# Optimization experiments

Measured on AMD Instinct MI355X. Metric: run time of the kernel, lower is better.

Reference implementation:

```python
import jax, jax.numpy as jnp
import numpy as np
import math

NUM_HEADS = 8
NUM_CHANNELS = 512
B, C, H, W = 8, 512, 32, 32
LN_EPS = 1e-6


def setup_inputs() -> dict:
    key = jax.random.key(0)
    ks = jax.random.split(key, 7)
    s = 1.0 / math.sqrt(NUM_CHANNELS)
    return {
        "key": jax.random.normal(ks[0], (B, C, H, W), jnp.float32),
        "value": jax.random.normal(ks[1], (B, C, H, W), jnp.float32),
        "query": jax.random.normal(ks[2], (B, C, H, W), jnp.float32),
        "Wq": jax.random.normal(ks[3], (C, C), jnp.float32) * s,
        "Wk": jax.random.normal(ks[4], (C, C), jnp.float32) * s,
        "Wv": jax.random.normal(ks[5], (C, C), jnp.float32) * s,
        "Wo": jax.random.normal(ks[6], (C, C), jnp.float32) * s,
        "ln_gamma": jnp.ones((C,), jnp.float32),
        "ln_beta": jnp.zeros((C,), jnp.float32),
    }


def _to_tokens(x):
    # b c h w -> b (h w) c
    b, c, h, w = x.shape
    return x.transpose(0, 2, 3, 1).reshape(b, h * w, c)


def _split_heads(x, m):
    # (B, HW, C) -> (B, m, HW, d); matches reshape (B,HW,m,d) then 'b hw m d -> (b m) hw d'
    b, hw, c = x.shape
    d = c // m
    return x.reshape(b, hw, m, d).transpose(0, 2, 1, 3)


def _merge_heads_cm(x):
    # (B, m, HW, d) -> (B, HW, d*m) with channel index = c*m + head  ('(b m) hw c -> b hw (c m)')
    b, m, hw, d = x.shape
    return x.transpose(0, 2, 3, 1).reshape(b, hw, d * m)


def reference(key, value, query, Wq, Wk, Wv, Wo, ln_gamma, ln_beta):
    m = NUM_HEADS
    b, c, h, w = query.shape
    d = c // m

    q = _to_tokens(query) @ Wq.T  # (B, HW, C)
    k = _to_tokens(key) @ Wk.T
    v = _to_tokens(value) @ Wv.T

    qh = _split_heads(q, m)  # (B, m, HW, d)
    kh = _split_heads(k, m)
    vh = _split_heads(v, m)

    scores = jnp.einsum('bmqd,bmkd->bmqk', qh, kh) / math.sqrt(d)
    p_attn = jax.nn.softmax(scores, axis=-1)
    out = jnp.einsum('bmqk,bmkd->bmqd', p_attn, vh)  # (B, m, HW, d)

    out = _merge_heads_cm(out)        # (B, HW, C) interleaved as (c m)
    residual = _merge_heads_cm(qh)    # same interleaving of projected query

    x = out + residual
    mu = jnp.mean(x, axis=-1, keepdims=True)
    var = jnp.mean(jnp.square(x - mu), axis=-1, keepdims=True)
    x = (x - mu) / jnp.sqrt(var + LN_EPS) * ln_gamma + ln_beta

    x = x @ Wo.T  # (B, HW, C)
    return x.reshape(b, h, w, c).transpose(0, 3, 1, 2)  # b (h w) c -> b c h w
```

## Files before the change

### kernel.cpp

```cpp
#include <hip/hip_runtime.h>
#include <stdint.h>

typedef __bf16 bf16x8 __attribute__((ext_vector_type(8)));
typedef float f32x4 __attribute__((ext_vector_type(4)));
typedef unsigned short u16x4 __attribute__((ext_vector_type(4)));
typedef unsigned short u16x8 __attribute__((ext_vector_type(8)));

#define MFMA16(a, b, c) __builtin_amdgcn_mfma_f32_16x16x32_bf16(a, b, c, 0, 0, 0)

__device__ __forceinline__ unsigned short f2bf(float f) {
  union { float f; unsigned u; } v; v.f = f;
  unsigned r = v.u + 0x7fffu + ((v.u >> 16) & 1u);
  return (unsigned short)(r >> 16);
}
__device__ __forceinline__ float bf2f(unsigned short h) {
  union { unsigned u; float f; } v; v.u = ((unsigned)h) << 16; return v.f;
}
__device__ __forceinline__ unsigned pk2(float a, float b) {
  union { unsigned u; __bf16 h[2]; } v;
  v.h[0] = (__bf16)a;
  v.h[1] = (__bf16)b;
  return v.u;
}
__device__ __forceinline__ void gload16(const void* g, void* l) {
  __builtin_amdgcn_global_load_lds(
      (const __attribute__((address_space(1))) void*)g,
      (__attribute__((address_space(3))) void*)l, 16, 0, 0);
}
__device__ __forceinline__ float fexp2(float x) {
#if __has_builtin(__builtin_amdgcn_exp2f)
  return __builtin_amdgcn_exp2f(x);
#else
  return exp2f(x);
#endif
}

__global__ __launch_bounds__(256) void prep_kernel(
    const float* __restrict__ q, const float* __restrict__ k,
    const float* __restrict__ v, unsigned short* __restrict__ oq,
    unsigned short* __restrict__ ok, unsigned short* __restrict__ ov,
    const float* __restrict__ w0, const float* __restrict__ w1,
    const float* __restrict__ w2, const float* __restrict__ w3,
    unsigned short* __restrict__ y0, unsigned short* __restrict__ y1,
    unsigned short* __restrict__ y2, unsigned short* __restrict__ y3) {
  __shared__ float tile[64][33];
  int z = blockIdx.z;
  if (z == 3) {
    int idx = blockIdx.y * 32 + blockIdx.x;
    if (idx >= 512) return;
    int wsel = idx >> 7, xb = idx & 127;
    const float* s = wsel == 0 ? w0 : wsel == 1 ? w1 : wsel == 2 ? w2 : w3;
    unsigned short* d = wsel == 0 ? y0 : wsel == 1 ? y1 : wsel == 2 ? y2 : y3;
    int t = xb * 256 + threadIdx.x;
    const f32x4* sp = (const f32x4*)(s + (size_t)t * 8);
    f32x4 a = sp[0], b = sp[1];
    u16x8 r;
    r[0] = f2bf(a[0]); r[1] = f2bf(a[1]); r[2] = f2bf(a[2]); r[3] = f2bf(a[3]);
    r[4] = f2bf(b[0]); r[5] = f2bf(b[1]); r[6] = f2bf(b[2]); r[7] = f2bf(b[3]);
    *(u16x8*)(d + (size_t)t * 8) = r;
    return;
  }
  const float* src = z == 0 ? q : z == 1 ? k : v;
  unsigned short* dst = z == 0 ? oq : z == 1 ? ok : ov;
  int bb = blockIdx.y >> 3;
  int c0 = (blockIdx.y & 7) * 64;
  int t0 = blockIdx.x * 32;
  int tx = threadIdx.x & 31, r = threadIdx.x >> 5;
#pragma unroll
  for (int i = 0; i < 8; ++i)
    tile[r + i * 8][tx] = src[(size_t)(bb * 512 + c0 + r + i * 8) * 1024 + t0 + tx];
  __syncthreads();
#pragma unroll
  for (int i = 0; i < 4; ++i) {
    int tr = r + i * 8;
    unsigned pack = (unsigned)f2bf(tile[2 * tx][tr]) |
                    ((unsigned)f2bf(tile[2 * tx + 1][tr]) << 16);
    *(unsigned*)(dst + (size_t)(bb * 1024 + t0 + tr) * 512 + c0 + 2 * tx) = pack;
  }
}

__global__ __launch_bounds__(256, 4) void gemm_qkv(
    const unsigned short* __restrict__ A0, const unsigned short* __restrict__ A1,
    const unsigned short* __restrict__ A2,
    const unsigned short* __restrict__ B0, const unsigned short* __restrict__ B1,
    const unsigned short* __restrict__ B2,
    unsigned short* __restrict__ O0, unsigned short* __restrict__ O1,
    unsigned short* __restrict__ O2) {
  __shared__ unsigned short aT[2][128 * 32];
  __shared__ unsigned short bT[2][128 * 32];
  int z = blockIdx.y;
  const unsigned short* A = z == 0 ? A0 : z == 1 ? A1 : A2;
  const unsigned short* BT = z == 0 ? B0 : z == 1 ? B1 : B2;
  int j = blockIdx.x;
  int bm = (j & 7) * 8 + (j >> 5);
  int bn = (j >> 3) & 3;
  int tid = threadIdx.x, lane = tid & 63, w = tid >> 6;
  int wr = w >> 1, wc = w & 1, l15 = lane & 15, lhi = lane >> 4;
  const int m0 = bm * 128, n0 = bn * 128;

  int u0 = tid, u1 = 256 + tid;
  int ar0 = u0 >> 2, ac0 = (u0 & 3) ^ (ar0 & 3);
  int ar1 = u1 >> 2, ac1 = (u1 & 3) ^ (ar1 & 3);
  const unsigned short* asrc0 = A + (size_t)(m0 + ar0) * 512 + ac0 * 8;
  const unsigned short* asrc1 = A + (size_t)(m0 + ar1) * 512 + ac1 * 8;
  const unsigned short* bsrc0 = BT + (size_t)(n0 + ar0) * 512 + ac0 * 8;
  const unsigned short* bsrc1 = BT + (size_t)(n0 + ar1) * 512 + ac1 * 8;

#define QSTAGE(bufi, it)                                     \
  do {                                                       \
    gload16(asrc0 + (it) * 32, &aT[bufi][u0 * 8]);           \
    gload16(asrc1 + (it) * 32, &aT[bufi][u1 * 8]);           \
    gload16(bsrc0 + (it) * 32, &bT[bufi][u0 * 8]);           \
    gload16(bsrc1 + (it) * 32, &bT[bufi][u1 * 8]);           \
  } while (0)

  int aoff[4], boff[4];
#pragma unroll
  for (int i = 0; i < 4; ++i) {
    int arow = wr * 64 + i * 16 + l15;
    int brow = wc * 64 + i * 16 + l15;
    aoff[i] = arow * 32 + ((lhi ^ (arow & 3)) * 8);
    boff[i] = brow * 32 + ((lhi ^ (brow & 3)) * 8);
  }

  f32x4 acc[4][4] = {};

#define QTILE(BUF, IT)                                                        \
  do {                                                                       \
    if ((IT) + 1 < 16) QSTAGE((BUF) ^ 1, (IT) + 1);                           \
    bf16x8 af[4], bfr[4];                                                    \
    _Pragma("unroll") for (int mi = 0; mi < 4; ++mi)                          \
        af[mi] = *(const bf16x8*)&aT[BUF][aoff[mi]];                          \
    _Pragma("unroll") for (int ni = 0; ni < 4; ++ni)                          \
        bfr[ni] = *(const bf16x8*)&bT[BUF][boff[ni]];                         \
    __builtin_amdgcn_s_setprio(1);                                           \
    _Pragma("unroll") for (int mi = 0; mi < 4; ++mi)                          \
        _Pragma("unroll") for (int ni = 0; ni < 4; ++ni)                      \
            acc[mi][ni] = MFMA16(af[mi], bfr[ni], acc[mi][ni]);               \
    __builtin_amdgcn_s_setprio(0);                                           \
    __syncthreads();                                                         \
  } while (0)

  QSTAGE(0, 0);
  __syncthreads();
  for (int it2 = 0; it2 < 16; it2 += 2) {
    QTILE(0, it2);
    QTILE(1, it2 + 1);
  }
#undef QTILE
#undef QSTAGE

  float sc = (z == 1) ? (0.125f * 1.44269504f) : 1.0f;
#pragma unroll
  for (int mi = 0; mi < 4; ++mi) {
#pragma unroll
    for (int ni = 0; ni < 4; ++ni) {
      int row = m0 + wr * 64 + mi * 16 + lhi * 4;
      int col = n0 + wc * 64 + ni * 16 + l15;
      if (z < 2) {
        unsigned short* C = z == 0 ? O0 : O1;
#pragma unroll
        for (int j2 = 0; j2 < 4; ++j2)
          C[(size_t)(row + j2) * 512 + col] = f2bf(acc[mi][ni][j2] * sc);
      } else {
        int bb = row >> 10, hw = row & 1023;
        u16x4 p;
        p[0] = f2bf(acc[mi][ni][0]); p[1] = f2bf(acc[mi][ni][1]);
        p[2] = f2bf(acc[mi][ni][2]); p[3] = f2bf(acc[mi][ni][3]);
        *(u16x4*)&O2[(size_t)bb * 524288 + (size_t)col * 1024 + hw] = p;
      }
    }
  }
}

__global__ __launch_bounds__(256, 4) void gemm_out(const unsigned short* __restrict__ A,
                                                   const unsigned short* __restrict__ BT,
                                                   float* __restrict__ C) {
  __shared__ unsigned short aT[2][128 * 32];
  __shared__ unsigned short bT[2][64 * 32];
  int j = blockIdx.x;
  int bm = (j & 7) * 8 + (j >> 6);
  int bn = (j >> 3) & 7;
  int tid = threadIdx.x, lane = tid & 63, w = tid >> 6;
  int l15 = lane & 15, lhi = lane >> 4;
  const int m0 = bm * 128, n0 = bn * 64;

  int u0 = tid, u1 = 256 + tid;
  int ar0 = u0 >> 2, ac0 = (u0 & 3) ^ (ar0 & 3);
  int ar1 = u1 >> 2, ac1 = (u1 & 3) ^ (ar1 & 3);
  const unsigned short* asrc0 = A + (size_t)(m0 + ar0) * 512 + ac0 * 8;
  const unsigned short* asrc1 = A + (size_t)(m0 + ar1) * 512 + ac1 * 8;
  const unsigned short* bsrc0 = BT + (size_t)(n0 + ar0) * 512 + ac0 * 8;

#define OSTAGE(bufi, it)                                     \
  do {                                                       \
    gload16(asrc0 + (it) * 32, &aT[bufi][u0 * 8]);           \
    gload16(asrc1 + (it) * 32, &aT[bufi][u1 * 8]);           \
    gload16(bsrc0 + (it) * 32, &bT[bufi][u0 * 8]);           \
  } while (0)

  int aoff[2], boff[4];
#pragma unroll
  for (int i = 0; i < 2; ++i) {
    int arow = w * 32 + i * 16 + l15;
    aoff[i] = arow * 32 + ((lhi ^ (arow & 3)) * 8);
  }
#pragma unroll
  for (int i = 0; i < 4; ++i) {
    int brow = i * 16 + l15;
    boff[i] = brow * 32 + ((lhi ^ (brow & 3)) * 8);
  }

  f32x4 acc[2][4] = {};

#define OTILE(BUF, IT)                                                        \
  do {                                                                       \
    if ((IT) + 1 < 16) OSTAGE((BUF) ^ 1, (IT) + 1);                           \
    bf16x8 af[2], bfr[4];                                                    \
    _Pragma("unroll") for (int mi = 0; mi < 2; ++mi)                          \
        af[mi] = *(const bf16x8*)&aT[BUF][aoff[mi]];                          \
    _Pragma("unroll") for (int ni = 0; ni < 4; ++ni)                          \
        bfr[ni] = *(const bf16x8*)&bT[BUF][boff[ni]];                         \
    __builtin_amdgcn_s_setprio(1);                                           \
    _Pragma("unroll") for (int mi = 0; mi < 2; ++mi)                          \
        _Pragma("unroll") for (int ni = 0; ni < 4; ++ni)                      \
            acc[mi][ni] = MFMA16(af[mi], bfr[ni], acc[mi][ni]);               \
    __builtin_amdgcn_s_setprio(0);                                           \
    __syncthreads();                                                         \
  } while (0)

  OSTAGE(0, 0);
  __syncthreads();
  for (int it2 = 0; it2 < 16; it2 += 2) {
    OTILE(0, it2);
    OTILE(1, it2 + 1);
  }
#undef OTILE
#undef OSTAGE

#pragma unroll
  for (int mi = 0; mi < 2; ++mi) {
#pragma unroll
    for (int ni = 0; ni < 4; ++ni) {
      int row = m0 + w * 32 + mi * 16 + lhi * 4;
      int col = n0 + ni * 16 + l15;
      int bb = row >> 10, hw = row & 1023;
      *(f32x4*)&C[(size_t)bb * 524288 + (size_t)col * 1024 + hw] = acc[mi][ni];
    }
  }
}

__global__ __launch_bounds__(256, 2) void attn_kernel(
    const unsigned short* __restrict__ q_tok, const unsigned short* __restrict__ k_tok,
    const unsigned short* __restrict__ v_cm, unsigned short* __restrict__ y_hm) {
  __shared__ unsigned short k_lds[2][64 * 64];
  __shared__ unsigned short v_lds[2][64 * 64];
  __shared__ unsigned short p_lds[4][2][16 * 64];

  int bid = blockIdx.x;
  int slot = bid >> 3;
  int bh = (bid & 7) * 8 + (slot >> 3);
  int qb = slot & 7;
  int h = bh & 7, b = bh >> 3;
  int tid = threadIdx.x;
  int lane = tid & 63, w = tid >> 6;
  int l15 = lane & 15, lhi = lane >> 4;

  const unsigned short* kbase = k_tok + (size_t)b * 524288 + h * 64;
  const unsigned short* vbase = v_cm + (size_t)b * 524288 + (size_t)h * 65536;

  int qglob0 = b * 1024 + qb * 128 + w * 32;
  bf16x8 qf[2][2];
#pragma unroll
  for (int sub = 0; sub < 2; ++sub) {
    const unsigned short* qp =
        q_tok + (size_t)(qglob0 + sub * 16 + l15) * 512 + h * 64 + lhi * 8;
    qf[sub][0] = *(const bf16x8*)qp;
    qf[sub][1] = *(const bf16x8*)(qp + 32);
  }

  bf16x8 ones;
#pragma unroll
  for (int i = 0; i < 8; ++i) ones[i] = (__bf16)1.0f;

  int u0 = tid, u1 = 256 + tid;
  int r0 = u0 >> 3, c0 = (u0 & 7) ^ (r0 & 7);
  int r1 = u1 >> 3, c1 = (u1 & 7) ^ (r1 & 7);
  const unsigned short* ksrc0 = kbase + (size_t)r0 * 512 + c0 * 8;
  const unsigned short* ksrc1 = kbase + (size_t)r1 * 512 + c1 * 8;
  const unsigned short* vsrc0 = vbase + (size_t)r0 * 1024 + c0 * 8;
  const unsigned short* vsrc1 = vbase + (size_t)r1 * 1024 + c1 * 8;

#define STAGE(bufi, kti)                                                    \
  do {                                                                      \
    gload16(ksrc0 + (size_t)(kti) * 32768, &k_lds[bufi][u0 * 8]);           \
    gload16(ksrc1 + (size_t)(kti) * 32768, &k_lds[bufi][u1 * 8]);           \
    gload16(vsrc0 + (kti) * 64, &v_lds[bufi][u0 * 8]);                      \
    gload16(vsrc1 + (kti) * 64, &v_lds[bufi][u1 * 8]);                      \
  } while (0)

  int kvoff[4][2];
#pragma unroll
  for (int nt = 0; nt < 4; ++nt) {
    int brow = nt * 16 + l15, sw = brow & 7;
    kvoff[nt][0] = brow * 64 + ((lhi ^ sw) * 8);
    kvoff[nt][1] = brow * 64 + (((4 + lhi) ^ sw) * 8);
  }

  char* pb = (char*)&p_lds[w][0][0];
  int p2 = (l15 & 7) << 1;
  char* pwr[2][4];
  const char* prd[2][2];
#pragma unroll
  for (int sub = 0; sub < 2; ++sub) {
#pragma unroll
    for (int nt = 0; nt < 4; ++nt)
      pwr[sub][nt] = pb + sub * 2048 + l15 * 128 + ((((nt << 2) | lhi) ^ p2) << 3);
#pragma unroll
    for (int kc = 0; kc < 2; ++kc)
      prd[sub][kc] = pb + sub * 2048 + l15 * 128 + ((((kc << 3) | (lhi << 1)) ^ p2) << 3);
  }

  f32x4 ls[2] = {{0.f, 0.f, 0.f, 0.f}, {0.f, 0.f, 0.f, 0.f}};
  f32x4 o[2][4] = {};

#define TILE(BUF, KT)                                                        \
  do {                                                                       \
    if ((KT) + 1 < 16) STAGE((BUF) ^ 1, (KT) + 1);                           \
    const unsigned short* kl = k_lds[BUF];                                   \
    const unsigned short* vl = v_lds[BUF];                                   \
    f32x4 st[2][4];                                                          \
    __builtin_amdgcn_s_setprio(1);                                           \
    _Pragma("unroll") for (int nt = 0; nt < 4; ++nt) {                       \
      bf16x8 kf0 = *(const bf16x8*)&kl[kvoff[nt][0]];                        \
      bf16x8 kf1 = *(const bf16x8*)&kl[kvoff[nt][1]];                        \
      _Pragma("unroll") for (int sub = 0; sub < 2; ++sub) {                  \
        f32x4 a = {0.f, 0.f, 0.f, 0.f};                                      \
        a = MFMA16(kf0, qf[sub][0], a);                                      \
        a = MFMA16(kf1, qf[sub][1], a);                                      \
        st[sub][nt] = a;                                                     \
      }                                                                      \
    }                                                                        \
    __builtin_amdgcn_s_setprio(0);                                           \
    bf16x8 vf[4][2];                                                         \
    _Pragma("unroll") for (int dt = 0; dt < 4; ++dt) {                       \
      vf[dt][0] = *(const bf16x8*)&vl[kvoff[dt][0]];                         \
      vf[dt][1] = *(const bf16x8*)&vl[kvoff[dt][1]];                         \
    }                                                                        \
    _Pragma("unroll") for (int sub = 0; sub < 2; ++sub) {                    \
      _Pragma("unroll") for (int nt = 0; nt < 4; ++nt) {                     \
        float e0 = fexp2(st[sub][nt][0]);                                    \
        float e1 = fexp2(st[sub][nt][1]);                                    \
        float e2 = fexp2(st[sub][nt][2]);                                    \
        float e3 = fexp2(st[sub][nt][3]);                                    \
        uint2 pk;                                                            \
        pk.x = pk2(e0, e1);                                                  \
        pk.y = pk2(e2, e3);                                                  \
        *(uint2*)pwr[sub][nt] = pk;                                          \
      }                                                                      \
    }                                                                        \
    asm volatile("" ::: "memory");                                          \
    bf16x8 pf[2][2];                                                         \
    _Pragma("unroll") for (int sub = 0; sub < 2; ++sub) {                    \
      pf[sub][0] = *(const bf16x8*)prd[sub][0];                              \
      pf[sub][1] = *(const bf16x8*)prd[sub][1];                              \
    }                                                                        \
    __builtin_amdgcn_s_setprio(1);                                           \
    _Pragma("unroll") for (int dt = 0; dt < 4; ++dt) {                       \
      _Pragma("unroll") for (int sub = 0; sub < 2; ++sub) {                  \
        o[sub][dt] = MFMA16(pf[sub][0], vf[dt][0], o[sub][dt]);              \
        o[sub][dt] = MFMA16(pf[sub][1], vf[dt][1], o[sub][dt]);              \
      }                                                                      \
    }                                                                        \
    _Pragma("unroll") for (int sub = 0; sub < 2; ++sub) {                    \
      ls[sub] = MFMA16(pf[sub][0], ones, ls[sub]);                           \
      ls[sub] = MFMA16(pf[sub][1], ones, ls[sub]);                           \
    }                                                                        \
    __builtin_amdgcn_s_setprio(0);                                           \
    __syncthreads();                                                         \
  } while (0)

  STAGE(0, 0);
  __syncthreads();
  for (int kt2 = 0; kt2 < 16; kt2 += 2) {
    TILE(0, kt2);
    TILE(1, kt2 + 1);
  }
#undef TILE
#undef STAGE

#pragma unroll
  for (int sub = 0; sub < 2; ++sub) {
    float inv[4];
#pragma unroll
    for (int r = 0; r < 4; ++r) inv[r] = 1.0f / ls[sub][r];
#pragma unroll
    for (int dt = 0; dt < 4; ++dt) {
#pragma unroll
      for (int r = 0; r < 4; ++r) {
        int q = qglob0 + sub * 16 + lhi * 4 + r;
        size_t idx = (size_t)q * 512 + h * 64 + dt * 16 + l15;
        float res = bf2f(q_tok[idx]);
        y_hm[idx] = f2bf(o[sub][dt][r] * inv[r] + res);
      }
    }
  }
}

__global__ __launch_bounds__(256) void ln_kernel(
    const unsigned short* __restrict__ y_hm,
    const float* __restrict__ gamma, const float* __restrict__ beta,
    unsigned short* __restrict__ xln) {
  __shared__ float y_s[512];
  __shared__ float red[8];
  int row = blockIdx.x;
  int t = threadIdx.x;
  float y0 = bf2f(y_hm[(size_t)row * 512 + t]);
  float y1 = bf2f(y_hm[(size_t)row * 512 + 256 + t]);
  y_s[t] = y0;
  y_s[t + 256] = y1;
  float s = y0 + y1, ss = y0 * y0 + y1 * y1;
#pragma unroll
  for (int msk = 1; msk < 64; msk <<= 1) {
    s += __shfl_xor(s, msk);
    ss += __shfl_xor(ss, msk);
  }
  int w = t >> 6, lane = t & 63;
  if (lane == 0) { red[w] = s; red[4 + w] = ss; }
  __syncthreads();
  s = (red[0] + red[1]) + (red[2] + red[3]);
  ss = (red[4] + red[5]) + (red[6] + red[7]);
  float mean = s * (1.0f / 512.0f);
  float var = ss * (1.0f / 512.0f) - mean * mean;
  float rstd = rsqrtf(var + 1e-6f);
  int c0 = t, c1 = t + 256;
  int p0 = ((c0 & 7) << 6) | (c0 >> 3);
  int p1 = ((c1 & 7) << 6) | (c1 >> 3);
  xln[(size_t)row * 512 + c0] = f2bf((y_s[p0] - mean) * rstd * gamma[c0] + beta[c0]);
  xln[(size_t)row * 512 + c1] = f2bf((y_s[p1] - mean) * rstd * gamma[c1] + beta[c1]);
}

extern "C" void kernel_launch(void* const* d_in, const int* in_sizes, int n_in,
                              void* d_out, int out_size, void* d_ws, size_t ws_size,
                              hipStream_t stream) {
  const float* key   = (const float*)d_in[0];
  const float* value = (const float*)d_in[1];
  const float* query = (const float*)d_in[2];
  const float* Wq = (const float*)d_in[3];
  const float* Wk = (const float*)d_in[4];
  const float* Wv = (const float*)d_in[5];
  const float* Wo = (const float*)d_in[6];
  const float* gamma = (const float*)d_in[7];
  const float* beta  = (const float*)d_in[8];

  char* ws = (char*)d_ws;
  unsigned short* Wq_b = (unsigned short*)(ws);
  unsigned short* Wk_b = Wq_b + 262144;
  unsigned short* Wv_b = Wk_b + 262144;
  unsigned short* Wo_b = Wv_b + 262144;
  unsigned short* qT    = (unsigned short*)(ws + (size_t)(2u)  * 1048576);
  unsigned short* kT    = (unsigned short*)(ws + (size_t)(10u) * 1048576);
  unsigned short* vT    = (unsigned short*)(ws + (size_t)(18u) * 1048576);
  unsigned short* q_tok = (unsigned short*)(ws + (size_t)(26u) * 1048576);
  unsigned short* k_tok = (unsigned short*)(ws + (size_t)(34u) * 1048576);
  unsigned short* v_cm  = (unsigned short*)(ws + (size_t)(42u) * 1048576);
  unsigned short* xln   = qT;
  unsigned short* y_hm  = (unsigned short*)d_out;

  prep_kernel<<<dim3(32, 64, 4), 256, 0, stream>>>(query, key, value, qT, kT, vT,
                                                   Wq, Wk, Wv, Wo,
                                                   Wq_b, Wk_b, Wv_b, Wo_b);
  gemm_qkv<<<dim3(256, 3), 256, 0, stream>>>(qT, kT, vT, Wq_b, Wk_b, Wv_b,
                                             q_tok, k_tok, v_cm);
  attn_kernel<<<512, 256, 0, stream>>>(q_tok, k_tok, v_cm, y_hm);
  ln_kernel<<<8192, 256, 0, stream>>>(y_hm, gamma, beta, xln);
  gemm_out<<<512, 256, 0, stream>>>(xln, Wo_b, (float*)d_out);
}
```

Before: 87.03 us.

## Fuse NCHW transpose and bf16 cast of activations into QKV GEMM loads

Removes the separate prep pass that transposed q/k/v from channel-major fp32 to token-major bf16. The QKV GEMM now streams fp32 channel-major tiles straight into LDS with async loads, using an XOR swizzle, and converts to bf16 while building MFMA fragments. This drops a full read/write round trip of the activations through the workspace. In exchange the GEMM moves twice the A-tile bytes, uses more LDS and conversion ALU work, and runs with lower occupancy (launch bound 3). The weight conversion now runs as a small standalone kernel, and pk2 uses manual round-to-nearest-even.

```diff
diff --git a/kernel.cpp b/kernel.cpp
--- a/kernel.cpp
+++ b/kernel.cpp
@@ -17,10 +17,10 @@
   union { unsigned u; float f; } v; v.u = ((unsigned)h) << 16; return v.f;
 }
 __device__ __forceinline__ unsigned pk2(float a, float b) {
-  union { unsigned u; __bf16 h[2]; } v;
-  v.h[0] = (__bf16)a;
-  v.h[1] = (__bf16)b;
-  return v.u;
+  union { float f; unsigned u; } x, y; x.f = a; y.f = b;
+  unsigned ra = x.u + 0x7fffu + ((x.u >> 16) & 1u);
+  unsigned rb = y.u + 0x7fffu + ((y.u >> 16) & 1u);
+  return (ra >> 16) | (rb & 0xffff0000u);
 }
 __device__ __forceinline__ void gload16(const void* g, void* l) {
   __builtin_amdgcn_global_load_lds(
@@ -35,61 +35,34 @@
 #endif
 }
 
-__global__ __launch_bounds__(256) void prep_kernel(
-    const float* __restrict__ q, const float* __restrict__ k,
-    const float* __restrict__ v, unsigned short* __restrict__ oq,
-    unsigned short* __restrict__ ok, unsigned short* __restrict__ ov,
+__global__ __launch_bounds__(256) void wconv_kernel(
     const float* __restrict__ w0, const float* __restrict__ w1,
     const float* __restrict__ w2, const float* __restrict__ w3,
-    unsigned short* __restrict__ y0, unsigned short* __restrict__ y1,
-    unsigned short* __restrict__ y2, unsigned short* __restrict__ y3) {
-  __shared__ float tile[64][33];
-  int z = blockIdx.z;
-  if (z == 3) {
-    int idx = blockIdx.y * 32 + blockIdx.x;
-    if (idx >= 512) return;
-    int wsel = idx >> 7, xb = idx & 127;
-    const float* s = wsel == 0 ? w0 : wsel == 1 ? w1 : wsel == 2 ? w2 : w3;
-    unsigned short* d = wsel == 0 ? y0 : wsel == 1 ? y1 : wsel == 2 ? y2 : y3;
-    int t = xb * 256 + threadIdx.x;
-    const f32x4* sp = (const f32x4*)(s + (size_t)t * 8);
-    f32x4 a = sp[0], b = sp[1];
-    u16x8 r;
-    r[0] = f2bf(a[0]); r[1] = f2bf(a[1]); r[2] = f2bf(a[2]); r[3] = f2bf(a[3]);
-    r[4] = f2bf(b[0]); r[5] = f2bf(b[1]); r[6] = f2bf(b[2]); r[7] = f2bf(b[3]);
-    *(u16x8*)(d + (size_t)t * 8) = r;
-    return;
-  }
-  const float* src = z == 0 ? q : z == 1 ? k : v;
-  unsigned short* dst = z == 0 ? oq : z == 1 ? ok : ov;
-  int bb = blockIdx.y >> 3;
-  int c0 = (blockIdx.y & 7) * 64;
-  int t0 = blockIdx.x * 32;
-  int tx = threadIdx.x & 31, r = threadIdx.x >> 5;
-#pragma unroll
-  for (int i = 0; i < 8; ++i)
-    tile[r + i * 8][tx] = src[(size_t)(bb * 512 + c0 + r + i * 8) * 1024 + t0 + tx];
-  __syncthreads();
-#pragma unroll
-  for (int i = 0; i < 4; ++i) {
-    int tr = r + i * 8;
-    unsigned pack = (unsigned)f2bf(tile[2 * tx][tr]) |
-                    ((unsigned)f2bf(tile[2 * tx + 1][tr]) << 16);
-    *(unsigned*)(dst + (size_t)(bb * 1024 + t0 + tr) * 512 + c0 + 2 * tx) = pack;
-  }
-}
-
-__global__ __launch_bounds__(256, 4) void gemm_qkv(
-    const unsigned short* __restrict__ A0, const unsigned short* __restrict__ A1,
-    const unsigned short* __restrict__ A2,
+    unsigned short* __restrict__ o0, unsigned short* __restrict__ o1,
+    unsigned short* __restrict__ o2, unsigned short* __restrict__ o3) {
+  int z = blockIdx.y;
+  const float* s = z == 0 ? w0 : z == 1 ? w1 : z == 2 ? w2 : w3;
+  unsigned short* d = z == 0 ? o0 : z == 1 ? o1 : z == 2 ? o2 : o3;
+  int t = blockIdx.x * 256 + threadIdx.x;
+  const f32x4* sp = (const f32x4*)(s + (size_t)t * 8);
+  f32x4 a = sp[0], b = sp[1];
+  u16x8 r;
+  r[0] = f2bf(a[0]); r[1] = f2bf(a[1]); r[2] = f2bf(a[2]); r[3] = f2bf(a[3]);
+  r[4] = f2bf(b[0]); r[5] = f2bf(b[1]); r[6] = f2bf(b[2]); r[7] = f2bf(b[3]);
+  *(u16x8*)(d + (size_t)t * 8) = r;
+}
+
+__global__ __launch_bounds__(256, 3) void gemm_qkv(
+    const float* __restrict__ X0, const float* __restrict__ X1,
+    const float* __restrict__ X2,
     const unsigned short* __restrict__ B0, const unsigned short* __restrict__ B1,
     const unsigned short* __restrict__ B2,
     unsigned short* __restrict__ O0, unsigned short* __restrict__ O1,
     unsigned short* __restrict__ O2) {
-  __shared__ unsigned short aT[2][128 * 32];
-  __shared__ unsigned short bT[2][128 * 32];
+  __shared__ float aTf[2][4096];
+  __shared__ unsigned short bT[2][4096];
   int z = blockIdx.y;
-  const unsigned short* A = z == 0 ? A0 : z == 1 ? A1 : A2;
+  const float* X = z == 0 ? X0 : z == 1 ? X1 : X2;
   const unsigned short* BT = z == 0 ? B0 : z == 1 ? B1 : B2;
   int j = blockIdx.x;
   int bm = (j & 7) * 8 + (j >> 5);
@@ -97,29 +70,46 @@
   int tid = threadIdx.x, lane = tid & 63, w = tid >> 6;
   int wr = w >> 1, wc = w & 1, l15 = lane & 15, lhi = lane >> 4;
   const int m0 = bm * 128, n0 = bn * 128;
-
+  const int b512 = (m0 >> 10) * 512;
+  const int hw0 = m0 & 1023;
+
+  const float* asf[4];
+  int adoff[4];
+#pragma unroll
+  for (int i = 0; i < 4; ++i) {
+    int u = i * 256 + tid;
+    int ch = u >> 5, pc = u & 31;
+    int lc = pc ^ ((ch >> 3) & 3);
+    asf[i] = X + (size_t)(b512 + ch) * 1024 + hw0 + lc * 4;
+    adoff[i] = u * 4;
+  }
   int u0 = tid, u1 = 256 + tid;
-  int ar0 = u0 >> 2, ac0 = (u0 & 3) ^ (ar0 & 3);
-  int ar1 = u1 >> 2, ac1 = (u1 & 3) ^ (ar1 & 3);
-  const unsigned short* asrc0 = A + (size_t)(m0 + ar0) * 512 + ac0 * 8;
-  const unsigned short* asrc1 = A + (size_t)(m0 + ar1) * 512 + ac1 * 8;
-  const unsigned short* bsrc0 = BT + (size_t)(n0 + ar0) * 512 + ac0 * 8;
-  const unsigned short* bsrc1 = BT + (size_t)(n0 + ar1) * 512 + ac1 * 8;
-
-#define QSTAGE(bufi, it)                                     \
-  do {                                                       \
-    gload16(asrc0 + (it) * 32, &aT[bufi][u0 * 8]);           \
-    gload16(asrc1 + (it) * 32, &aT[bufi][u1 * 8]);           \
-    gload16(bsrc0 + (it) * 32, &bT[bufi][u0 * 8]);           \
-    gload16(bsrc1 + (it) * 32, &bT[bufi][u1 * 8]);           \
-  } while (0)
-
-  int aoff[4], boff[4];
+  int br0 = u0 >> 2, bc0 = (u0 & 3) ^ (br0 & 3);
+  int br1 = u1 >> 2, bc1 = (u1 & 3) ^ (br1 & 3);
+  const unsigned short* bsrc0 = BT + (size_t)(n0 + br0) * 512 + bc0 * 8;
+  const unsigned short* bsrc1 = BT + (size_t)(n0 + br1) * 512 + bc1 * 8;
+
+#define QSTAGE(bufi, it)                                            \
+  do {                                                              \
+    gload16(asf[0] + (it) * 32768, &aTf[bufi][adoff[0]]);           \
+    gload16(asf[1] + (it) * 32768, &aTf[bufi][adoff[1]]);           \
+    gload16(asf[2] + (it) * 32768, &aTf[bufi][adoff[2]]);           \
+    gload16(asf[3] + (it) * 32768, &aTf[bufi][adoff[3]]);           \
+    gload16(bsrc0 + (it) * 32, &bT[bufi][u0 * 8]);                  \
+    gload16(bsrc1 + (it) * 32, &bT[bufi][u1 * 8]);                  \
+  } while (0)
+
+  int aoffA[4];
+#pragma unroll
+  for (int mi = 0; mi < 4; ++mi) {
+    int tok = wr * 64 + mi * 16 + l15;
+    int atok = ((((tok >> 2) ^ lhi) << 2) | (tok & 3));
+    aoffA[mi] = lhi * 1024 + atok;
+  }
+  int boff[4];
 #pragma unroll
   for (int i = 0; i < 4; ++i) {
-    int arow = wr * 64 + i * 16 + l15;
     int brow = wc * 64 + i * 16 + l15;
-    aoff[i] = arow * 32 + ((lhi ^ (arow & 3)) * 8);
     boff[i] = brow * 32 + ((lhi ^ (brow & 3)) * 8);
   }
 
@@ -129,8 +119,20 @@
   do {                                                                       \
     if ((IT) + 1 < 16) QSTAGE((BUF) ^ 1, (IT) + 1);                           \
     bf16x8 af[4], bfr[4];                                                    \
-    _Pragma("unroll") for (int mi = 0; mi < 4; ++mi)                          \
-        af[mi] = *(const bf16x8*)&aT[BUF][aoff[mi]];                          \
+    _Pragma("unroll") for (int mi = 0; mi < 4; ++mi) {                        \
+      union { unsigned u[4]; bf16x8 v; } ap;                                  \
+      float a0 = aTf[BUF][aoffA[mi] + 0 * 128];                               \
+      float a1 = aTf[BUF][aoffA[mi] + 1 * 128];                               \
+      float a2 = aTf[BUF][aoffA[mi] + 2 * 128];                               \
+      float a3 = aTf[BUF][aoffA[mi] + 3 * 128];                               \
+      float a4 = aTf[BUF][aoffA[mi] + 4 * 128];                               \
+      float a5 = aTf[BUF][aoffA[mi] + 5 * 128];                               \
+      float a6 = aTf[BUF][aoffA[mi] + 6 * 128];                               \
+      float a7 = aTf[BUF][aoffA[mi] + 7 * 128];                               \
+      ap.u[0] = pk2(a0, a1); ap.u[1] = pk2(a2, a3);                           \
+      ap.u[2] = pk2(a4, a5); ap.u[3] = pk2(a6, a7);                           \
+      af[mi] = ap.v;                                                          \
+    }                                                                         \
     _Pragma("unroll") for (int ni = 0; ni < 4; ++ni)                          \
         bfr[ni] = *(const bf16x8*)&bT[BUF][boff[ni]];                         \
     __builtin_amdgcn_s_setprio(1);                                           \
@@ -458,19 +460,14 @@
   unsigned short* Wk_b = Wq_b + 262144;
   unsigned short* Wv_b = Wk_b + 262144;
   unsigned short* Wo_b = Wv_b + 262144;
-  unsigned short* qT    = (unsigned short*)(ws + (size_t)(2u)  * 1048576);
-  unsigned short* kT    = (unsigned short*)(ws + (size_t)(10u) * 1048576);
-  unsigned short* vT    = (unsigned short*)(ws + (size_t)(18u) * 1048576);
   unsigned short* q_tok = (unsigned short*)(ws + (size_t)(26u) * 1048576);
   unsigned short* k_tok = (unsigned short*)(ws + (size_t)(34u) * 1048576);
   unsigned short* v_cm  = (unsigned short*)(ws + (size_t)(42u) * 1048576);
-  unsigned short* xln   = qT;
+  unsigned short* xln   = (unsigned short*)(ws + (size_t)(2u) * 1048576);
   unsigned short* y_hm  = (unsigned short*)d_out;
 
-  prep_kernel<<<dim3(32, 64, 4), 256, 0, stream>>>(query, key, value, qT, kT, vT,
-                                                   Wq, Wk, Wv, Wo,
-                                                   Wq_b, Wk_b, Wv_b, Wo_b);
-  gemm_qkv<<<dim3(256, 3), 256, 0, stream>>>(qT, kT, vT, Wq_b, Wk_b, Wv_b,
+  wconv_kernel<<<dim3(128, 4), 256, 0, stream>>>(Wq, Wk, Wv, Wo, Wq_b, Wk_b, Wv_b, Wo_b);
+  gemm_qkv<<<dim3(256, 3), 256, 0, stream>>>(query, key, value, Wq_b, Wk_b, Wv_b,
                                              q_tok, k_tok, v_cm);
   attn_kernel<<<512, 256, 0, stream>>>(q_tok, k_tok, v_cm, y_hm);
   ln_kernel<<<8192, 256, 0, stream>>>(y_hm, gamma, beta, xln);
```

After: 87.15 us. About the same (+0.1%).
